# Kernel optimization log

Hardware: AMD Instinct MI355X
Metric: run time of the kernel (lower is better)

The kernel has to match this reference:

```python
import jax, jax.numpy as jnp
import numpy as np

NT, NTR, NQ = 2048, 4096, 257  # time samples, traces, quantile knots


def cumtrapz(y, dx):
    # cumulative trapezoid along last axis, zero-prepended (preserve_dims=True)
    c = jnp.cumsum((y[..., 1:] + y[..., :-1]) * (0.5 * dx), axis=-1)
    return jnp.concatenate([jnp.zeros_like(y[..., :1]), c], axis=-1)


def trapz(y, dx):
    return (jnp.sum(y, axis=-1) - 0.5 * (y[..., 0] + y[..., -1])) * dx


def renorm(f, dx):
    # square + normalize to a pdf along time (standard W2-FWI renormalization)
    g = f * f
    return g / trapz(g, dx)[..., None]


def true_quantile(pdf, x, p, dx):
    # step-function quantile: invert clipped CDF via searchsorted per trace
    cdf = jnp.clip(cumtrapz(pdf, dx), 0.0, 1.0)  # [B, nt]
    idx = jax.vmap(lambda c: jnp.searchsorted(c, p))(cdf)  # [B, nq]
    idx = jnp.clip(idx, 0, x.shape[0] - 1)
    return x[idx]  # [B, nq]


def natural_cubic_coeffs(p, q):
    # batched natural cubic spline of q(p); knots p shared across batch
    h = p[1:] - p[:-1]                                 # [n-1]
    slope = (q[..., 1:] - q[..., :-1]) / h             # [B, n-1]
    rhs = 6.0 * (slope[..., 1:] - slope[..., :-1])     # [B, n-2]
    diag = 2.0 * (h[:-1] + h[1:])
    off = h[1:-1]
    T = jnp.diag(diag) + jnp.diag(off, 1) + jnp.diag(off, -1)  # [n-2, n-2], shared
    M_inner = jnp.linalg.solve(T, rhs[..., None])[..., 0]      # [B, n-2]
    z = jnp.zeros_like(q[..., :1])
    M = jnp.concatenate([z, M_inner, z], axis=-1)      # natural BCs: M0 = Mn = 0
    a = q[..., :-1]
    b = slope - h * (2.0 * M[..., :-1] + M[..., 1:]) / 6.0
    c = 0.5 * M[..., :-1]
    d = (M[..., 1:] - M[..., :-1]) / (6.0 * h)
    return a, b, c, d  # each [B, n-1]


def spline_eval(p, a, b, c, d, tq):
    # vectorized batched spline evaluation (replaces per-element Python loop)
    idx = jnp.clip(jnp.searchsorted(p, tq, side='left') - 1, 0, p.shape[0] - 2)
    frac = tq - p[idx]
    ga = jnp.take_along_axis(a, idx, axis=-1)
    gb = jnp.take_along_axis(b, idx, axis=-1)
    gc = jnp.take_along_axis(c, idx, axis=-1)
    gd = jnp.take_along_axis(d, idx, axis=-1)
    return ga + frac * (gb + frac * (gc + frac * gd))


def w2_forward(f, obs_data, t, p):
    dx = t[1] - t[0]
    # constructor-time part: quantile splines of observed data
    q = true_quantile(renorm(obs_data, dx), t, p, dx)   # [B, nq]
    a, b, c, d = natural_cubic_coeffs(p, q)
    # forward: CDF of synthetic, composed with observed quantile
    F = cumtrapz(renorm(f, dx), dx)                     # [B, nt]
    off_diag = spline_eval(p, a, b, c, d, F)            # [B, nt]
    diff = (t[None, :] - off_diag) ** 2
    integrated = trapz(diff * f, dx)                    # [B]
    return jnp.sum(integrated)


def setup_inputs() -> dict:
    key = jax.random.key(0)
    k1, k2 = jax.random.split(key)
    f = jax.random.normal(k1, (NTR, NT), dtype=jnp.float32)
    obs_data = jax.random.normal(k2, (NTR, NT), dtype=jnp.float32)
    t = jnp.linspace(0.0, 2.0, NT, dtype=jnp.float32)
    p = jnp.linspace(0.0, 1.0, NQ, dtype=jnp.float32)
    return {"f": f, "obs_data": obs_data, "t": t, "p": p}


def reference(f, obs_data, t, p):
    return w2_forward(f, obs_data, t, p)
```

## Files before the change

### kernel.cpp

```cpp
#include <hip/hip_runtime.h>

#define TPB 256
#define NT_ 2048
#define NQ_ 257
#define EPT 8
#define BW 8
#define BD (2*BW+1)
#define H_P 0.00390625f
#define RTPB 1024

struct Band { float v[BD * 256]; };
constexpr Band make_band() {
  Band b{};
  double L[256] = {}, winv[256] = {};
  const double H = 1.0 / 256.0;
  double w = 4.0 * H;
  winv[0] = 1.0 / w;
  L[0] = 0.0;
  for (int i = 1; i < 255; i++) {
    L[i] = H * winv[i - 1];
    w = 4.0 * H - L[i] * H;
    winv[i] = 1.0 / w;
  }
  for (int j = 0; j < 255; j++) {
    double y[BW + 1] = {};
    y[0] = 1.0;
    for (int m = 1; m <= BW; m++) {
      int i = j + m;
      y[m] = (i <= 254) ? (-L[i] * y[m - 1]) : 0.0;
    }
    double xn = 0.0;
    for (int m = BW; m >= 0; m--) {
      int i = j + m;
      double val = 0.0;
      if (i <= 254) {
        double num = y[m] - ((i < 254) ? H * xn : 0.0);
        val = num * winv[i];
        xn = val;
      }
      b.v[(m + BW) * 256 + j] = (float)val;
    }
    for (int m = -1; m >= -BW; m--) {
      int i = j + m;
      double val = 0.0;
      if (i >= 0) {
        val = (-H * xn) * winv[i];
        xn = val;
      }
      b.v[(m + BW) * 256 + j] = (float)val;
    }
  }
  return b;
}
__device__ __constant__ Band g_band = make_band();

__device__ __forceinline__ double shfl_down_f64(double x, int off) {
  union { double d; int i[2]; } u; u.d = x;
  u.i[0] = __shfl_down(u.i[0], off, 64);
  u.i[1] = __shfl_down(u.i[1], off, 64);
  return u.d;
}

template<int CTRL, int RM, int BM, bool BC>
__device__ __forceinline__ float dppf(float x) {
  return __int_as_float(__builtin_amdgcn_update_dpp(
      0, __float_as_int(x), CTRL, RM, BM, BC));
}
template<int CTRL, int RM, int BM, bool BC>
__device__ __forceinline__ double dppd(double x) {
  union { double d; int i[2]; } u, o; u.d = x;
  o.i[0] = __builtin_amdgcn_update_dpp(0, u.i[0], CTRL, RM, BM, BC);
  o.i[1] = __builtin_amdgcn_update_dpp(0, u.i[1], CTRL, RM, BM, BC);
  return o.d;
}
__device__ __forceinline__ void iscan2(float& a, float& b) {
  a += dppf<0x111,0xF,0xF,true >(a);  b += dppf<0x111,0xF,0xF,true >(b);
  a += dppf<0x112,0xF,0xF,true >(a);  b += dppf<0x112,0xF,0xF,true >(b);
  a += dppf<0x114,0xF,0xF,true >(a);  b += dppf<0x114,0xF,0xF,true >(b);
  a += dppf<0x118,0xF,0xF,true >(a);  b += dppf<0x118,0xF,0xF,true >(b);
  a += dppf<0x142,0xa,0xF,false>(a);  b += dppf<0x142,0xa,0xF,false>(b);
  a += dppf<0x143,0xc,0xF,false>(a);  b += dppf<0x143,0xc,0xF,false>(b);
}
__device__ __forceinline__ void iscan2d(double& a, double& b) {
  a += dppd<0x111,0xF,0xF,true >(a);  b += dppd<0x111,0xF,0xF,true >(b);
  a += dppd<0x112,0xF,0xF,true >(a);  b += dppd<0x112,0xF,0xF,true >(b);
  a += dppd<0x114,0xF,0xF,true >(a);  b += dppd<0x114,0xF,0xF,true >(b);
  a += dppd<0x118,0xF,0xF,true >(a);  b += dppd<0x118,0xF,0xF,true >(b);
  a += dppd<0x142,0xa,0xF,false>(a);  b += dppd<0x142,0xa,0xF,false>(b);
  a += dppd<0x143,0xc,0xF,false>(a);  b += dppd<0x143,0xc,0xF,false>(b);
}

__global__ __launch_bounds__(TPB) void w2_main(
    const float* __restrict__ f, const float* __restrict__ obs,
    const float* __restrict__ t, double* __restrict__ row_out) {
  __shared__ float s_qA[NQ_], s_qB[NQ_];
  __shared__ float s_rhsA[255 + 2 * BW], s_rhsB[255 + 2 * BW];
  __shared__ float s_MA[NQ_], s_MB[NQ_];
  __shared__ float4 s_coefA[256], s_coefB[256];
  __shared__ float s_wfA[4], s_wfB[4], s_wf2A[4], s_wf2B[4];
  __shared__ double s_wdA[4], s_wdB[4];
  __shared__ double s_miscA[2], s_miscB[2];

  const int tid = threadIdx.x;
  const int lane = tid & 63;
  const int wid = tid >> 6;
  const int rowA = (int)blockIdx.x * 2;
  const int rowB = rowA + 1;
  const int base = tid * EPT;
  const int emax = (tid == TPB - 1) ? EPT - 1 : EPT;

  const double dx = (double)t[1] - (double)t[0];

  float tl[EPT + 1];
  {
    const float4 a = *reinterpret_cast<const float4*>(t + base);
    const float4 b = *reinterpret_cast<const float4*>(t + base + 4);
    tl[0] = a.x; tl[1] = a.y; tl[2] = a.z; tl[3] = a.w;
    tl[4] = b.x; tl[5] = b.y; tl[6] = b.z; tl[7] = b.w;
  }
  tl[EPT] = (tid < TPB - 1) ? t[base + EPT] : 0.0f;

  float sAA[EPT], sAB[EPT];
  float epA = 0.0f, epB = 0.0f;
  {
    const float* orA = obs + (size_t)rowA * NT_;
    const float* orB = obs + (size_t)rowB * NT_;
    float ovA[EPT + 1], ovB[EPT + 1];
    {
      const float4 a0 = *reinterpret_cast<const float4*>(orA + base);
      const float4 a1 = *reinterpret_cast<const float4*>(orA + base + 4);
      const float4 b0 = *reinterpret_cast<const float4*>(orB + base);
      const float4 b1 = *reinterpret_cast<const float4*>(orB + base + 4);
      ovA[0] = a0.x; ovA[1] = a0.y; ovA[2] = a0.z; ovA[3] = a0.w;
      ovA[4] = a1.x; ovA[5] = a1.y; ovA[6] = a1.z; ovA[7] = a1.w;
      ovB[0] = b0.x; ovB[1] = b0.y; ovB[2] = b0.z; ovB[3] = b0.w;
      ovB[4] = b1.x; ovB[5] = b1.y; ovB[6] = b1.z; ovB[7] = b1.w;
    }
    ovA[EPT] = (tid < TPB - 1) ? orA[base + EPT] : 0.0f;
    ovB[EPT] = (tid < TPB - 1) ? orB[base + EPT] : 0.0f;
    for (int k = 0; k < emax; k++) {
      sAA[k] = ovA[k] * ovA[k] + ovA[k + 1] * ovA[k + 1];
      sAB[k] = ovB[k] * ovB[k] + ovB[k + 1] * ovB[k + 1];
      epA += sAA[k];
      epB += sAB[k];
    }
    if (emax < EPT) { sAA[EPT - 1] = 0.0f; sAB[EPT - 1] = 0.0f; }
  }
  float vA = epA, vB = epB;
  iscan2(vA, vB);
  float exclA = __shfl_up(vA, 1, 64);
  float exclB = __shfl_up(vB, 1, 64);
  if (lane == 0) { exclA = 0.0f; exclB = 0.0f; }
  if (lane == 63) { s_wfA[wid] = vA; s_wfB[wid] = vB; }
  __syncthreads();
  float woffA = 0.0f, totA = 0.0f, woffB = 0.0f, totB = 0.0f;
  #pragma unroll
  for (int w = 0; w < 4; w++) {
    float swA = s_wfA[w], swB = s_wfB[w];
    if (w < wid) { woffA += swA; woffB += swB; }
    totA += swA; totB += swB;
  }
  float runA = woffA + exclA, inclA = woffA + vA, invA = 1.0f / totA;
  float runB = woffB + exclB, inclB = woffB + vB, invB = 1.0f / totB;

  {
    float cprev = fminf(runA * invA, 1.0f);
    int j = (int)(cprev * 256.0f) + 1;
    float r = runA;
    for (int k = 0; k < emax; k++) {
      float cu_uns = (k == emax - 1) ? inclA : (r + sAA[k]);
      r = cu_uns;
      float cuc = fminf(cu_uns * invA, 1.0f);
      int jh = (int)(cuc * 256.0f);
      float tq = tl[k + 1];
      for (; j <= jh; j++) s_qA[j] = tq;
    }
    if (tid == 0) s_qA[0] = tl[0];
    if (tid == TPB - 1) {
      float tq = tl[EPT - 1];
      for (; j <= 256; j++) s_qA[j] = tq;
    }
  }
  {
    float cprev = fminf(runB * invB, 1.0f);
    int j = (int)(cprev * 256.0f) + 1;
    float r = runB;
    for (int k = 0; k < emax; k++) {
      float cu_uns = (k == emax - 1) ? inclB : (r + sAB[k]);
      r = cu_uns;
      float cuc = fminf(cu_uns * invB, 1.0f);
      int jh = (int)(cuc * 256.0f);
      float tq = tl[k + 1];
      for (; j <= jh; j++) s_qB[j] = tq;
    }
    if (tid == 0) s_qB[0] = tl[0];
    if (tid == TPB - 1) {
      float tq = tl[EPT - 1];
      for (; j <= 256; j++) s_qB[j] = tq;
    }
  }

  const float* frA = f + (size_t)rowA * NT_;
  const float* frB = f + (size_t)rowB * NT_;
  float fvA[EPT + 1], fvB[EPT + 1];
  {
    const float4 a0 = *reinterpret_cast<const float4*>(frA + base);
    const float4 a1 = *reinterpret_cast<const float4*>(frA + base + 4);
    const float4 b0 = *reinterpret_cast<const float4*>(frB + base);
    const float4 b1 = *reinterpret_cast<const float4*>(frB + base + 4);
    fvA[0] = a0.x; fvA[1] = a0.y; fvA[2] = a0.z; fvA[3] = a0.w;
    fvA[4] = a1.x; fvA[5] = a1.y; fvA[6] = a1.z; fvA[7] = a1.w;
    fvB[0] = b0.x; fvB[1] = b0.y; fvB[2] = b0.z; fvB[3] = b0.w;
    fvB[4] = b1.x; fvB[5] = b1.y; fvB[6] = b1.z; fvB[7] = b1.w;
  }
  fvA[EPT] = (tid < TPB - 1) ? frA[base + EPT] : 0.0f;
  fvB[EPT] = (tid < TPB - 1) ? frB[base + EPT] : 0.0f;

  float sBA[EPT], sBB[EPT];
  float ep2A = 0.0f, ep2B = 0.0f;
  for (int k = 0; k < emax; k++) {
    sBA[k] = fvA[k] * fvA[k] + fvA[k + 1] * fvA[k + 1];
    sBB[k] = fvB[k] * fvB[k] + fvB[k + 1] * fvB[k + 1];
    ep2A += sBA[k];
    ep2B += sBB[k];
  }
  if (emax < EPT) { sBA[EPT - 1] = 0.0f; sBB[EPT - 1] = 0.0f; }
  float v2A = ep2A, v2B = ep2B;
  iscan2(v2A, v2B);
  float excl2A = __shfl_up(v2A, 1, 64);
  float excl2B = __shfl_up(v2B, 1, 64);
  if (lane == 0) { excl2A = 0.0f; excl2B = 0.0f; }
  if (lane == 63) { s_wf2A[wid] = v2A; s_wf2B[wid] = v2B; }
  __syncthreads();

  float woff2A = 0.0f, tot2A = 0.0f, woff2B = 0.0f, tot2B = 0.0f;
  #pragma unroll
  for (int w = 0; w < 4; w++) {
    float swA = s_wf2A[w], swB = s_wf2B[w];
    if (w < wid) { woff2A += swA; woff2B += swB; }
    tot2A += swA; tot2B += swB;
  }
  float run2A = woff2A + excl2A, inv2A = 1.0f / tot2A;
  float run2B = woff2B + excl2B, inv2B = 1.0f / tot2B;

  if (tid < 255) {
    float sl0A = (s_qA[tid + 1] - s_qA[tid]) * 256.0f;
    float sl1A = (s_qA[tid + 2] - s_qA[tid + 1]) * 256.0f;
    s_rhsA[BW + tid] = 6.0f * (sl1A - sl0A);
    float sl0B = (s_qB[tid + 1] - s_qB[tid]) * 256.0f;
    float sl1B = (s_qB[tid + 2] - s_qB[tid + 1]) * 256.0f;
    s_rhsB[BW + tid] = 6.0f * (sl1B - sl0B);
  }
  if (tid < BW) { s_rhsA[tid] = 0.0f; s_rhsB[tid] = 0.0f; }
  if (tid >= TPB - BW) {
    s_rhsA[tid + (2 * BW - 1)] = 0.0f;
    s_rhsB[tid + (2 * BW - 1)] = 0.0f;
  }
  __syncthreads();

  float MregA = 0.0f, MregB = 0.0f;
  if (tid < 255) {
    #pragma unroll
    for (int dd = 0; dd < BD; dd++) {
      float w = g_band.v[dd * 256 + tid];
      MregA += w * s_rhsA[tid + dd];
      MregB += w * s_rhsB[tid + dd];
    }
  }
  if (tid < 255) { s_MA[tid + 1] = MregA; s_MB[tid + 1] = MregB; }
  if (tid == 0) { s_MA[0] = 0.0f; s_MA[256] = 0.0f; s_MB[0] = 0.0f; s_MB[256] = 0.0f; }
  __syncthreads();

  {
    const float h = H_P;
    float q0A = s_qA[tid], q1A = s_qA[tid + 1];
    float MiA = s_MA[tid], Mi1A = s_MA[tid + 1];
    float slA = (q1A - q0A) * 256.0f;
    float bA = slA - h * (2.0f * MiA + Mi1A) * (1.0f / 6.0f);
    s_coefA[tid] = make_float4(q0A, bA, 0.5f * MiA, (Mi1A - MiA) * (256.0f / 6.0f));
    float q0B = s_qB[tid], q1B = s_qB[tid + 1];
    float MiB = s_MB[tid], Mi1B = s_MB[tid + 1];
    float slB = (q1B - q0B) * 256.0f;
    float bB = slB - h * (2.0f * MiB + Mi1B) * (1.0f / 6.0f);
    s_coefB[tid] = make_float4(q0B, bB, 0.5f * MiB, (Mi1B - MiB) * (256.0f / 6.0f));
  }
  __syncthreads();

  float csumA = 0.0f, csumB = 0.0f;
  {
    float r2A = run2A, r2B = run2B;
    #pragma unroll
    for (int k = 0; k < EPT; k++) {
      if (k > 0) { r2A += sBA[k - 1]; r2B += sBB[k - 1]; }
      float FA = r2A * inv2A;
      float FB = r2B * inv2B;
      int idxA = (int)ceilf(FA * 256.0f) - 1;
      int idxB = (int)ceilf(FB * 256.0f) - 1;
      if (idxA < 0) idxA = 0; if (idxA > 255) idxA = 255;
      if (idxB < 0) idxB = 0; if (idxB > 255) idxB = 255;
      float fracA = FA - (float)idxA * H_P;
      float fracB = FB - (float)idxB * H_P;
      float4 cfA = s_coefA[idxA];
      float4 cfB = s_coefB[idxB];
      float valA = cfA.x + fracA * (cfA.y + fracA * (cfA.z + fracA * cfA.w));
      float valB = cfB.x + fracB * (cfB.y + fracB * (cfB.z + fracB * cfB.w));
      float diffA = tl[k] - valA;
      float diffB = tl[k] - valB;
      float wvA = diffA * diffA * fvA[k];
      float wvB = diffB * diffB * fvB[k];
      if (tid == 0 && k == 0) { s_miscA[0] = (double)wvA; s_miscB[0] = (double)wvB; }
      if (tid == TPB - 1 && k == EPT - 1) { s_miscA[1] = (double)wvA; s_miscB[1] = (double)wvB; }
      csumA += wvA;
      csumB += wvB;
    }
  }
  double rA = (double)csumA, rB = (double)csumB;
  iscan2d(rA, rB);
  if (lane == 63) { s_wdA[wid] = rA; s_wdB[wid] = rB; }
  __syncthreads();
  if (tid == 0) {
    double totwA = s_wdA[0] + s_wdA[1] + s_wdA[2] + s_wdA[3];
    double totwB = s_wdB[0] + s_wdB[1] + s_wdB[2] + s_wdB[3];
    row_out[rowA] = (totwA - 0.5 * (s_miscA[0] + s_miscA[1])) * dx;
    row_out[rowB] = (totwB - 0.5 * (s_miscB[0] + s_miscB[1])) * dx;
  }
}

__global__ __launch_bounds__(RTPB) void w2_reduce(const double* __restrict__ row_out,
                                                  int ntr, float* __restrict__ out) {
  __shared__ double s[RTPB / 64];
  int tid = threadIdx.x, lane = tid & 63, wid = tid >> 6;
  double v = 0.0;
  for (int i = tid; i < ntr; i += RTPB) v += row_out[i];
  #pragma unroll
  for (int off = 32; off >= 1; off >>= 1) v += shfl_down_f64(v, off);
  if (lane == 0) s[wid] = v;
  __syncthreads();
  if (tid == 0) {
    double tot = 0.0;
    #pragma unroll
    for (int i = 0; i < RTPB / 64; i++) tot += s[i];
    out[0] = (float)tot;
  }
}

extern "C" void kernel_launch(void* const* d_in, const int* in_sizes, int n_in,
                              void* d_out, int out_size, void* d_ws, size_t ws_size,
                              hipStream_t stream) {
  const float* f   = (const float*)d_in[0];
  const float* obs = (const float*)d_in[1];
  const float* t   = (const float*)d_in[2];
  int nt = in_sizes[2];
  int ntr = in_sizes[0] / nt;

  double* rows = (double*)d_ws;

  hipLaunchKernelGGL(w2_main, dim3(ntr / 2), dim3(TPB), 0, stream,
                     f, obs, t, rows);
  hipLaunchKernelGGL(w2_reduce, dim3(1), dim3(RTPB), 0, stream,
                     rows, ntr, (float*)d_out);
}
```

Measured before the change: 36.29 us.

## Fold spline RHS into banded solve weights, use shuffles for neighbor moments

```diff
diff --git a/kernel.cpp b/kernel.cpp
--- a/kernel.cpp
+++ b/kernel.cpp
@@ -4,50 +4,65 @@
 #define NT_ 2048
 #define NQ_ 257
 #define EPT 8
-#define BW 8
-#define BD (2*BW+1)
+#define BWQ 5
+#define BWS (BWQ + 2)
+#define BD2 (2*BWQ + 3)
+#define PQ BWQ
+#define QLEN (PQ + NQ_ + BWQ + 2)
 #define H_P 0.00390625f
 #define RTPB 1024
 
-struct Band { float v[BD * 256]; };
+struct Band { float v[BD2 * 256]; };
 constexpr Band make_band() {
   Band b{};
   double L[256] = {}, winv[256] = {};
   const double H = 1.0 / 256.0;
-  double w = 4.0 * H;
-  winv[0] = 1.0 / w;
+  winv[0] = 1.0 / (4.0 * H);
   L[0] = 0.0;
   for (int i = 1; i < 255; i++) {
     L[i] = H * winv[i - 1];
-    w = 4.0 * H - L[i] * H;
-    winv[i] = 1.0 / w;
-  }
-  for (int j = 0; j < 255; j++) {
-    double y[BW + 1] = {};
+    winv[i] = 1.0 / (4.0 * H - L[i] * H);
+  }
+  for (int i = 0; i < 255; i++) {
+    double col[2 * BWS + 1] = {};
+    double y[BWS + 1] = {};
     y[0] = 1.0;
-    for (int m = 1; m <= BW; m++) {
-      int i = j + m;
-      y[m] = (i <= 254) ? (-L[i] * y[m - 1]) : 0.0;
+    for (int m = 1; m <= BWS; m++) {
+      int idx = i + m;
+      y[m] = (idx <= 254) ? (-L[idx] * y[m - 1]) : 0.0;
     }
     double xn = 0.0;
-    for (int m = BW; m >= 0; m--) {
-      int i = j + m;
+    for (int m = BWS; m >= 0; m--) {
+      int idx = i + m;
       double val = 0.0;
-      if (i <= 254) {
-        double num = y[m] - ((i < 254) ? H * xn : 0.0);
-        val = num * winv[i];
+      if (idx <= 254) {
+        double num = y[m] - ((idx < 254) ? H * xn : 0.0);
+        val = num * winv[idx];
         xn = val;
       }
-      b.v[(m + BW) * 256 + j] = (float)val;
-    }
-    for (int m = -1; m >= -BW; m--) {
-      int i = j + m;
+      col[m + BWS] = val;
+    }
+    for (int m = -1; m >= -BWS; m--) {
+      int idx = i + m;
       double val = 0.0;
-      if (i >= 0) {
-        val = (-H * xn) * winv[i];
+      if (idx >= 0) {
+        val = (-H * xn) * winv[idx];
         xn = val;
       }
-      b.v[(m + BW) * 256 + j] = (float)val;
+      col[m + BWS] = val;
+    }
+    for (int mm = 0; mm < BD2; mm++) {
+      int n = i - BWQ + mm;
+      double w = 0.0;
+      if (n >= 0 && n <= 256) {
+        double s0 = 0.0, s1 = 0.0, s2 = 0.0;
+        int d0 = n - i, d1 = n - 1 - i, d2 = n - 2 - i;
+        if (n     >= 0 && n     <= 254 && d0 >= -BWS && d0 <= BWS) s0 = col[d0 + BWS];
+        if (n - 1 >= 0 && n - 1 <= 254 && d1 >= -BWS && d1 <= BWS) s1 = col[d1 + BWS];
+        if (n - 2 >= 0 && n - 2 <= 254 && d2 >= -BWS && d2 <= BWS) s2 = col[d2 + BWS];
+        w = 1536.0 * (s0 - 2.0 * s1 + s2);
+      }
+      b.v[mm * 256 + i] = (float)w;
     }
   }
   return b;
@@ -93,9 +108,7 @@
 __global__ __launch_bounds__(TPB) void w2_main(
     const float* __restrict__ f, const float* __restrict__ obs,
     const float* __restrict__ t, double* __restrict__ row_out) {
-  __shared__ float s_qA[NQ_], s_qB[NQ_];
-  __shared__ float s_rhsA[255 + 2 * BW], s_rhsB[255 + 2 * BW];
-  __shared__ float s_MA[NQ_], s_MB[NQ_];
+  __shared__ float s_qA[QLEN], s_qB[QLEN];
   __shared__ float4 s_coefA[256], s_coefB[256];
   __shared__ float s_wfA[4], s_wfB[4], s_wf2A[4], s_wf2B[4];
   __shared__ double s_wdA[4], s_wdB[4];
@@ -110,6 +123,12 @@
   const int emax = (tid == TPB - 1) ? EPT - 1 : EPT;
 
   const double dx = (double)t[1] - (double)t[0];
+
+  if (tid < PQ) { s_qA[tid] = 0.0f; s_qB[tid] = 0.0f; }
+  if (tid >= TPB - (BWQ + 2)) {
+    int o = PQ + NQ_ + tid - (TPB - (BWQ + 2));
+    s_qA[o] = 0.0f; s_qB[o] = 0.0f;
+  }
 
   float tl[EPT + 1];
   {
@@ -160,43 +179,45 @@
     if (w < wid) { woffA += swA; woffB += swB; }
     totA += swA; totB += swB;
   }
-  float runA = woffA + exclA, inclA = woffA + vA, invA = 1.0f / totA;
-  float runB = woffB + exclB, inclB = woffB + vB, invB = 1.0f / totB;
-
-  {
-    float cprev = fminf(runA * invA, 1.0f);
-    int j = (int)(cprev * 256.0f) + 1;
+  float runA = woffA + exclA, inclA = woffA + vA;
+  float runB = woffB + exclB, inclB = woffB + vB;
+  float invA256 = 256.0f / totA;
+  float invB256 = 256.0f / totB;
+
+  {
+    float cprevS = fminf(runA * invA256, 256.0f);
+    int j = (int)cprevS + 1;
     float r = runA;
     for (int k = 0; k < emax; k++) {
       float cu_uns = (k == emax - 1) ? inclA : (r + sAA[k]);
       r = cu_uns;
-      float cuc = fminf(cu_uns * invA, 1.0f);
-      int jh = (int)(cuc * 256.0f);
+      float cuS = fminf(cu_uns * invA256, 256.0f);
+      int jh = (int)cuS;
       float tq = tl[k + 1];
-      for (; j <= jh; j++) s_qA[j] = tq;
-    }
-    if (tid == 0) s_qA[0] = tl[0];
+      for (; j <= jh; j++) s_qA[PQ + j] = tq;
+    }
+    if (tid == 0) s_qA[PQ + 0] = tl[0];
     if (tid == TPB - 1) {
       float tq = tl[EPT - 1];
-      for (; j <= 256; j++) s_qA[j] = tq;
-    }
-  }
-  {
-    float cprev = fminf(runB * invB, 1.0f);
-    int j = (int)(cprev * 256.0f) + 1;
+      for (; j <= 256; j++) s_qA[PQ + j] = tq;
+    }
+  }
+  {
+    float cprevS = fminf(runB * invB256, 256.0f);
+    int j = (int)cprevS + 1;
     float r = runB;
     for (int k = 0; k < emax; k++) {
       float cu_uns = (k == emax - 1) ? inclB : (r + sAB[k]);
       r = cu_uns;
-      float cuc = fminf(cu_uns * invB, 1.0f);
-      int jh = (int)(cuc * 256.0f);
+      float cuS = fminf(cu_uns * invB256, 256.0f);
+      int jh = (int)cuS;
       float tq = tl[k + 1];
-      for (; j <= jh; j++) s_qB[j] = tq;
-    }
-    if (tid == 0) s_qB[0] = tl[0];
+      for (; j <= jh; j++) s_qB[PQ + j] = tq;
+    }
+    if (tid == 0) s_qB[PQ + 0] = tl[0];
     if (tid == TPB - 1) {
       float tq = tl[EPT - 1];
-      for (; j <= 256; j++) s_qB[j] = tq;
+      for (; j <= 256; j++) s_qB[PQ + j] = tq;
     }
   }
 
@@ -240,49 +261,43 @@
     if (w < wid) { woff2A += swA; woff2B += swB; }
     tot2A += swA; tot2B += swB;
   }
-  float run2A = woff2A + excl2A, inv2A = 1.0f / tot2A;
-  float run2B = woff2B + excl2B, inv2B = 1.0f / tot2B;
-
-  if (tid < 255) {
-    float sl0A = (s_qA[tid + 1] - s_qA[tid]) * 256.0f;
-    float sl1A = (s_qA[tid + 2] - s_qA[tid + 1]) * 256.0f;
-    s_rhsA[BW + tid] = 6.0f * (sl1A - sl0A);
-    float sl0B = (s_qB[tid + 1] - s_qB[tid]) * 256.0f;
-    float sl1B = (s_qB[tid + 2] - s_qB[tid + 1]) * 256.0f;
-    s_rhsB[BW + tid] = 6.0f * (sl1B - sl0B);
-  }
-  if (tid < BW) { s_rhsA[tid] = 0.0f; s_rhsB[tid] = 0.0f; }
-  if (tid >= TPB - BW) {
-    s_rhsA[tid + (2 * BW - 1)] = 0.0f;
-    s_rhsB[tid + (2 * BW - 1)] = 0.0f;
-  }
-  __syncthreads();
+  float run2A = woff2A + excl2A, inv2A256 = 256.0f / tot2A;
+  float run2B = woff2B + excl2B, inv2B256 = 256.0f / tot2B;
 
   float MregA = 0.0f, MregB = 0.0f;
   if (tid < 255) {
     #pragma unroll
-    for (int dd = 0; dd < BD; dd++) {
-      float w = g_band.v[dd * 256 + tid];
-      MregA += w * s_rhsA[tid + dd];
-      MregB += w * s_rhsB[tid + dd];
-    }
-  }
-  if (tid < 255) { s_MA[tid + 1] = MregA; s_MB[tid + 1] = MregB; }
-  if (tid == 0) { s_MA[0] = 0.0f; s_MA[256] = 0.0f; s_MB[0] = 0.0f; s_MB[256] = 0.0f; }
-  __syncthreads();
+    for (int mm = 0; mm < BD2; mm++) {
+      float w = g_band.v[mm * 256 + tid];
+      MregA += w * s_qA[tid + mm];
+      MregB += w * s_qB[tid + mm];
+    }
+  }
+  float MprevA = __shfl_up(MregA, 1, 64);
+  float MprevB = __shfl_up(MregB, 1, 64);
+  if (lane == 63) { s_wfA[wid] = MregA; s_wfB[wid] = MregB; }
+  __syncthreads();
+  if (lane == 0) {
+    MprevA = (wid == 0) ? 0.0f : s_wfA[wid - 1];
+    MprevB = (wid == 0) ? 0.0f : s_wfB[wid - 1];
+  }
 
   {
     const float h = H_P;
-    float q0A = s_qA[tid], q1A = s_qA[tid + 1];
-    float MiA = s_MA[tid], Mi1A = s_MA[tid + 1];
+    float q0A = s_qA[PQ + tid], q1A = s_qA[PQ + tid + 1];
     float slA = (q1A - q0A) * 256.0f;
-    float bA = slA - h * (2.0f * MiA + Mi1A) * (1.0f / 6.0f);
-    s_coefA[tid] = make_float4(q0A, bA, 0.5f * MiA, (Mi1A - MiA) * (256.0f / 6.0f));
-    float q0B = s_qB[tid], q1B = s_qB[tid + 1];
-    float MiB = s_MB[tid], Mi1B = s_MB[tid + 1];
+    float bA = slA - h * (2.0f * MprevA + MregA) * (1.0f / 6.0f);
+    float cA = 0.5f * MprevA;
+    float dA = (MregA - MprevA) * (256.0f / 6.0f);
+    s_coefA[tid] = make_float4(q0A, bA * (1.0f / 256.0f),
+                               cA * (1.0f / 65536.0f), dA * (1.0f / 16777216.0f));
+    float q0B = s_qB[PQ + tid], q1B = s_qB[PQ + tid + 1];
     float slB = (q1B - q0B) * 256.0f;
-    float bB = slB - h * (2.0f * MiB + Mi1B) * (1.0f / 6.0f);
-    s_coefB[tid] = make_float4(q0B, bB, 0.5f * MiB, (Mi1B - MiB) * (256.0f / 6.0f));
+    float bB = slB - h * (2.0f * MprevB + MregB) * (1.0f / 6.0f);
+    float cB = 0.5f * MprevB;
+    float dB = (MregB - MprevB) * (256.0f / 6.0f);
+    s_coefB[tid] = make_float4(q0B, bB * (1.0f / 256.0f),
+                               cB * (1.0f / 65536.0f), dB * (1.0f / 16777216.0f));
   }
   __syncthreads();
 
@@ -292,18 +307,20 @@
     #pragma unroll
     for (int k = 0; k < EPT; k++) {
       if (k > 0) { r2A += sBA[k - 1]; r2B += sBB[k - 1]; }
-      float FA = r2A * inv2A;
-      float FB = r2B * inv2B;
-      int idxA = (int)ceilf(FA * 256.0f) - 1;
-      int idxB = (int)ceilf(FB * 256.0f) - 1;
-      if (idxA < 0) idxA = 0; if (idxA > 255) idxA = 255;
-      if (idxB < 0) idxB = 0; if (idxB > 255) idxB = 255;
-      float fracA = FA - (float)idxA * H_P;
-      float fracB = FB - (float)idxB * H_P;
+      float GA = r2A * inv2A256;
+      float GB = r2B * inv2B256;
+      float fiA = ceilf(GA) - 1.0f;
+      float fiB = ceilf(GB) - 1.0f;
+      fiA = fminf(fmaxf(fiA, 0.0f), 255.0f);
+      fiB = fminf(fmaxf(fiB, 0.0f), 255.0f);
+      int idxA = (int)fiA;
+      int idxB = (int)fiB;
+      float uA = GA - fiA;
+      float uB = GB - fiB;
       float4 cfA = s_coefA[idxA];
       float4 cfB = s_coefB[idxB];
-      float valA = cfA.x + fracA * (cfA.y + fracA * (cfA.z + fracA * cfA.w));
-      float valB = cfB.x + fracB * (cfB.y + fracB * (cfB.z + fracB * cfB.w));
+      float valA = cfA.x + uA * (cfA.y + uA * (cfA.z + uA * cfA.w));
+      float valB = cfB.x + uB * (cfB.y + uB * (cfB.z + uB * cfB.w));
       float diffA = tl[k] - valA;
       float diffB = tl[k] - valB;
       float wvA = diffA * diffA * fvA[k];
```

New measurement: 35.80 us. Within noise of the previous version (-1.4%).
